# Optimization experiments

Hardware: AMD Instinct MI355X
Metric: run time of the kernel (lower is better)

Reference implementation:

```python
import jax, jax.numpy as jnp
import numpy as np

EMBED = 2048
HEADS = 16
HEAD_DIM = EMBED // HEADS


def setup_inputs() -> dict:
    key = jax.random.key(0)
    ks = jax.random.split(key, 9)
    s = 1.0 / np.sqrt(EMBED)
    inp = {"x": jax.random.normal(ks[0], (2, 2048, EMBED), dtype=jnp.float32)}
    for i, name in enumerate(["q", "k", "v", "o"]):
        inp[f"W{name}"] = jax.random.uniform(ks[1 + 2 * i], (EMBED, EMBED), dtype=jnp.float32, minval=-s, maxval=s)
        inp[f"b{name}"] = jax.random.uniform(ks[2 + 2 * i], (EMBED,), dtype=jnp.float32, minval=-s, maxval=s)
    return inp


def reference(x, Wq, bq, Wk, bk, Wv, bv, Wo, bo):
    B, S, E = x.shape
    def split_heads(t):
        return t.reshape(B, S, HEADS, HEAD_DIM).transpose(0, 2, 1, 3)  # [B,H,S,D]
    q = split_heads(x @ Wq.T + bq)
    k = split_heads(x @ Wk.T + bk)
    v = split_heads(x @ Wv.T + bv)
    scale = 1.0 / np.sqrt(HEAD_DIM)
    scores = jnp.einsum("bhqd,bhkd->bhqk", q, k) * scale  # [B,H,S,S]
    causal = jnp.tril(jnp.ones((S, S), dtype=bool))
    scores = jnp.where(causal[None, None], scores, -jnp.inf)
    attn = jax.nn.softmax(scores, axis=-1)
    out = jnp.einsum("bhqk,bhkd->bhqd", attn, v)  # [B,H,S,D]
    out = out.transpose(0, 2, 1, 3).reshape(B, S, E)
    return out @ Wo.T + bo
```

## Files before the change

### kernel.cpp

```cpp
#include <hip/hip_runtime.h>

typedef unsigned short u16;
typedef unsigned int u32;
typedef __attribute__((ext_vector_type(8))) short bf16x8;
typedef __attribute__((ext_vector_type(4))) float f32x4;

#define MFMA(a, b, c) __builtin_amdgcn_mfma_f32_16x16x32_bf16((a), (b), (c), 0, 0, 0)

__device__ inline u16 f2bf(float f) {
  u32 u = __float_as_uint(f);
  u = (u + 0x7fffu + ((u >> 16) & 1u)) >> 16;
  return (u16)u;
}

__device__ inline void gld16(u16* lds, const u16* g) {
  __builtin_amdgcn_global_load_lds((const __attribute__((address_space(1))) void*)g,
                                   (__attribute__((address_space(3))) void*)lds,
                                   16, 0, 0);
}

__global__ __launch_bounds__(256) void cvt_all(const float* __restrict__ x,
                                               const float* __restrict__ wa,
                                               const float* __restrict__ wb,
                                               const float* __restrict__ wc,
                                               const float* __restrict__ wd,
                                               uint2* __restrict__ dst) {
  int i = blockIdx.x * 256 + threadIdx.x;
  const float* s;
  int off;
  if (i < 2097152) {
    s = x; off = i;
  } else {
    int j = i - 2097152;
    int which = j >> 20;
    off = j & 1048575;
    s = (which == 0) ? wa : (which == 1) ? wb : (which == 2) ? wc : wd;
  }
  float4 f = ((const float4*)s)[off];
  u32 lo = (u32)f2bf(f.x) | ((u32)f2bf(f.y) << 16);
  u32 hi = (u32)f2bf(f.z) | ((u32)f2bf(f.w) << 16);
  dst[i] = make_uint2(lo, hi);
}

__device__ inline void gemm_core(const u16* __restrict__ A, const u16* __restrict__ W,
                                 u16* As, u16* Bs, int m0, int n0, f32x4 acc[4][4]) {
  const int K = 2048;
  const int NT = 64;
  int t = threadIdx.x, w = t >> 6, l = t & 63;
  int wr = (w >> 1) * 64, wc = (w & 1) * 64;
  int fr = l & 15, fg = l >> 4;
  int r0 = t >> 2;
  int r1 = 64 + r0;
  int c00 = (t & 3) ^ ((r0 >> 1) & 3);
  int c01 = (t & 3) ^ ((r1 >> 1) & 3);
  const u16* gA = A + (size_t)m0 * K;
  const u16* gB = W + (size_t)n0 * K;
  size_t a0 = (size_t)r0 * K + c00 * 8;
  size_t a1 = (size_t)r1 * K + c01 * 8;
#pragma unroll
  for (int p = 0; p < 2; ++p) {
    u16* sa = As + p * 4096;
    u16* sb = Bs + p * 4096;
    int kk = p * 32;
    gld16(sa + w * 512, gA + a0 + kk);
    gld16(sa + 2048 + w * 512, gA + a1 + kk);
    gld16(sb + w * 512, gB + a0 + kk);
    gld16(sb + 2048 + w * 512, gB + a1 + kk);
  }
  for (int kt = 0; kt < NT; ++kt) {
    int kt2 = (kt + 2 < NT) ? (kt + 2) : (NT - 1);
    u16* sa = As + ((kt + 2) & 3) * 4096;
    u16* sb = Bs + ((kt + 2) & 3) * 4096;
    int kk = kt2 * 32;
    gld16(sa + w * 512, gA + a0 + kk);
    gld16(sa + 2048 + w * 512, gA + a1 + kk);
    gld16(sb + w * 512, gB + a0 + kk);
    gld16(sb + 2048 + w * 512, gB + a1 + kk);
    asm volatile("s_waitcnt vmcnt(8)\n\ts_barrier" ::: "memory");
    const u16* ca = As + (kt & 3) * 4096;
    const u16* cb = Bs + (kt & 3) * 4096;
    bf16x8 af[4], bfv[4];
#pragma unroll
    for (int i = 0; i < 4; ++i) {
      int ar = wr + i * 16 + fr;
      af[i] = *(const bf16x8*)&ca[ar * 32 + ((fg ^ ((ar >> 1) & 3)) << 3)];
    }
#pragma unroll
    for (int i = 0; i < 4; ++i) {
      int br = wc + i * 16 + fr;
      bfv[i] = *(const bf16x8*)&cb[br * 32 + ((fg ^ ((br >> 1) & 3)) << 3)];
    }
    __builtin_amdgcn_s_setprio(1);
#pragma unroll
    for (int mi = 0; mi < 4; ++mi)
#pragma unroll
      for (int ni = 0; ni < 4; ++ni)
        acc[mi][ni] = MFMA(af[mi], bfv[ni], acc[mi][ni]);
    __builtin_amdgcn_s_setprio(0);
  }
}

__global__ __launch_bounds__(512, 2) void qk_gemm(
    const u16* __restrict__ X, const u16* __restrict__ Wq, const u16* __restrict__ Wk,
    const float* __restrict__ bq, const float* __restrict__ bk, u16* __restrict__ Qo,
    u16* __restrict__ Ko) {
  __shared__ __attribute__((aligned(16))) u16 As[32768];
  __shared__ __attribute__((aligned(16))) u16 Bs[32768];
  const int K = 2048, NT = 64;
  int which = blockIdx.x >> 3;
  int n0 = (blockIdx.x & 7) * 256;
  int m0 = blockIdx.y * 256;
  const u16* W = (which == 0) ? Wq : Wk;
  const float* bias = (which == 0) ? bq : bk;
  u16* out = (which == 0) ? Qo : Ko;
  float scale = (which == 0) ? 0.08838834764831845f : 1.0f;
  int t = threadIdx.x, w = t >> 6, l = t & 63;
  int wm = w >> 2, wn = w & 3;
  int fr = l & 15, fg = l >> 4;
  int r0 = t >> 2;
  int c0 = (t & 3) ^ ((r0 >> 1) & 3);
  const u16* gA = X + (size_t)m0 * K;
  const u16* gB = W + (size_t)n0 * K;
  size_t a0 = (size_t)r0 * K + c0 * 8;
  size_t a1 = a0 + (size_t)128 * K;
  f32x4 zero4 = {0.f, 0.f, 0.f, 0.f};
  f32x4 acc[8][4];
#pragma unroll
  for (int i = 0; i < 8; ++i)
#pragma unroll
    for (int j = 0; j < 4; ++j) acc[i][j] = zero4;
#pragma unroll
  for (int p = 0; p < 2; ++p) {
    u16* sa = As + p * 8192;
    u16* sb = Bs + p * 8192;
    int kk = p * 32;
    gld16(sa + w * 512, gA + a0 + kk);
    gld16(sa + 4096 + w * 512, gA + a1 + kk);
    gld16(sb + w * 512, gB + a0 + kk);
    gld16(sb + 4096 + w * 512, gB + a1 + kk);
  }
  for (int kt = 0; kt < NT; ++kt) {
    int kt2 = (kt + 2 < NT) ? (kt + 2) : (NT - 1);
    u16* sa = As + ((kt + 2) & 3) * 8192;
    u16* sb = Bs + ((kt + 2) & 3) * 8192;
    int kk = kt2 * 32;
    gld16(sa + w * 512, gA + a0 + kk);
    gld16(sa + 4096 + w * 512, gA + a1 + kk);
    gld16(sb + w * 512, gB + a0 + kk);
    gld16(sb + 4096 + w * 512, gB + a1 + kk);
    asm volatile("s_waitcnt vmcnt(8)\n\ts_barrier" ::: "memory");
    const u16* ca = As + (kt & 3) * 8192;
    const u16* cb = Bs + (kt & 3) * 8192;
    bf16x8 af[8], bfv[4];
#pragma unroll
    for (int i = 0; i < 8; ++i) {
      int ar = wm * 128 + i * 16 + fr;
      af[i] = *(const bf16x8*)&ca[ar * 32 + ((fg ^ ((ar >> 1) & 3)) << 3)];
    }
#pragma unroll
    for (int i = 0; i < 4; ++i) {
      int br = wn * 64 + i * 16 + fr;
      bfv[i] = *(const bf16x8*)&cb[br * 32 + ((fg ^ ((br >> 1) & 3)) << 3)];
    }
    __builtin_amdgcn_s_setprio(1);
#pragma unroll
    for (int mi = 0; mi < 8; ++mi)
#pragma unroll
      for (int ni = 0; ni < 4; ++ni)
        acc[mi][ni] = MFMA(af[mi], bfv[ni], acc[mi][ni]);
    __builtin_amdgcn_s_setprio(0);
  }
#pragma unroll
  for (int mi = 0; mi < 8; ++mi) {
#pragma unroll
    for (int ni = 0; ni < 4; ++ni) {
      int row = m0 + wm * 128 + mi * 16 + (l >> 4) * 4;
      int col = n0 + wn * 64 + ni * 16 + (l & 15);
      float bb = bias[col];
      int h = col >> 7, d = col & 127;
#pragma unroll
      for (int i = 0; i < 4; ++i) {
        int m = row + i;
        int b = m >> 11, s = m & 2047;
        float v = (acc[mi][ni][i] + bb) * scale;
        out[(((size_t)b * 16 + h) * 2048 + s) * 128 + d] = f2bf(v);
      }
    }
  }
}

__global__ __launch_bounds__(256, 2) void v_gemm(const u16* __restrict__ X,
                                                 const u16* __restrict__ Wv,
                                                 const float* __restrict__ bv,
                                                 u16* __restrict__ Vo) {
  __shared__ __attribute__((aligned(16))) u16 As[16384];
  __shared__ __attribute__((aligned(16))) u16 Bs[16384];
  int n0 = blockIdx.x * 128, m0 = blockIdx.y * 128;
  f32x4 zero4 = {0.f, 0.f, 0.f, 0.f};
  f32x4 acc[4][4];
#pragma unroll
  for (int i = 0; i < 4; ++i)
#pragma unroll
    for (int j = 0; j < 4; ++j) acc[i][j] = zero4;
  gemm_core(X, Wv, As, Bs, m0, n0, acc);
  int t = threadIdx.x, w = t >> 6, l = t & 63;
  int wr = (w >> 1) * 64, wc = (w & 1) * 64;
#pragma unroll
  for (int mi = 0; mi < 4; ++mi) {
#pragma unroll
    for (int ni = 0; ni < 4; ++ni) {
      int row = m0 + wr + mi * 16 + (l >> 4) * 4;
      int col = n0 + wc + ni * 16 + (l & 15);
      float bb = bv[col];
      int h = col >> 7, d = col & 127;
      int b = row >> 11, s = row & 2047;
      u32 p0 = (u32)f2bf(acc[mi][ni][0] + bb) | ((u32)f2bf(acc[mi][ni][1] + bb) << 16);
      u32 p1 = (u32)f2bf(acc[mi][ni][2] + bb) | ((u32)f2bf(acc[mi][ni][3] + bb) << 16);
      *(uint2*)&Vo[((size_t)(b * 16 + h) * 128 + d) * 2048 + s] = make_uint2(p0, p1);
    }
  }
}

__global__ __launch_bounds__(256, 2) void oproj_gemm(const u16* __restrict__ A,
                                                     const u16* __restrict__ W,
                                                     const float* __restrict__ bias,
                                                     float* __restrict__ out) {
  __shared__ __attribute__((aligned(16))) u16 As[16384];
  __shared__ __attribute__((aligned(16))) u16 Bs[16384];
  int n0 = blockIdx.x * 128, m0 = blockIdx.y * 128;
  f32x4 zero4 = {0.f, 0.f, 0.f, 0.f};
  f32x4 acc[4][4];
#pragma unroll
  for (int i = 0; i < 4; ++i)
#pragma unroll
    for (int j = 0; j < 4; ++j) acc[i][j] = zero4;
  gemm_core(A, W, As, Bs, m0, n0, acc);
  int t = threadIdx.x, w = t >> 6, l = t & 63;
  int wr = (w >> 1) * 64, wc = (w & 1) * 64;
#pragma unroll
  for (int mi = 0; mi < 4; ++mi) {
#pragma unroll
    for (int ni = 0; ni < 4; ++ni) {
      int row = m0 + wr + mi * 16 + (l >> 4) * 4;
      int col = n0 + wc + ni * 16 + (l & 15);
      float bb = bias[col];
#pragma unroll
      for (int i = 0; i < 4; ++i) out[(size_t)(row + i) * 2048 + col] = acc[mi][ni][i] + bb;
    }
  }
}

__global__ __launch_bounds__(256, 2) void attn_fwd(const u16* __restrict__ Q,
                                                   const u16* __restrict__ K,
                                                   const u16* __restrict__ Vt,
                                                   u16* __restrict__ AO) {
  __shared__ __attribute__((aligned(16))) u16 Ks[16384];
  __shared__ __attribute__((aligned(16))) u16 Vts[16384];
  __shared__ __attribute__((aligned(16))) u16 Pl[8192];
  const int D = 128;
  int b3 = blockIdx.x;
  int bh = b3 & 31;
  int xq = b3 >> 5;
  int qt = (xq < 8) ? (15 - xq) : (xq - 8);
  int t = threadIdx.x, w = t >> 6, l = t & 63, g = l >> 4, c = l & 15;
  size_t base = (size_t)bh * 2048 * 128;
  const u16* Vbh = Vt + base;
  int q0 = qt * 128;
  int qrw = q0 + w * 32;
  bf16x8 qf[2][4];
#pragma unroll
  for (int mi = 0; mi < 2; ++mi) {
    const u16* qp = Q + base + (size_t)(qrw + mi * 16 + c) * D + g * 8;
#pragma unroll
    for (int ks = 0; ks < 4; ++ks) qf[mi][ks] = *(const bf16x8*)(qp + ks * 32);
  }
  f32x4 zero4 = {0.f, 0.f, 0.f, 0.f};
  f32x4 oacc[2][8];
#pragma unroll
  for (int mi = 0; mi < 2; ++mi)
#pragma unroll
    for (int i = 0; i < 8; ++i) oacc[mi][i] = zero4;
  float mrow[2][4], lrow[2][4];
#pragma unroll
  for (int mi = 0; mi < 2; ++mi)
#pragma unroll
    for (int i = 0; i < 4; ++i) { mrow[mi][i] = -1e30f; lrow[mi][i] = 0.f; }
  char* pw = (char*)(Pl + w * 2048);
  int ktmax = 2 * qt + 1;
#define STAGE_TILE(BUF, KV0)                                                          \
  {                                                                                   \
    _Pragma("unroll") for (int ci = 0; ci < 4; ++ci) {                                \
      int row = w * 16 + ci * 4 + g;                                                  \
      int cc = c ^ (row & 7);                                                         \
      gld16(Ks + (BUF)*8192 + w * 2048 + ci * 512,                                    \
            K + base + (size_t)((KV0) + row) * D + cc * 8);                           \
    }                                                                                 \
    _Pragma("unroll") for (int ci = 0; ci < 4; ++ci) {                                \
      int vr = ci * 32 + w * 8 + (l >> 3);                                            \
      int vslot = (l & 7) ^ ((l >> 3) & 7);                                           \
      gld16(Vts + (BUF)*8192 + ci * 2048 + w * 512,                                   \
            Vbh + (size_t)vr * 2048 + (KV0) + vslot * 8);                             \
    }                                                                                 \
  }
  STAGE_TILE(0, 0)
  for (int kt = 0; kt <= ktmax; ++kt) {
    int kv0 = kt * 64;
    int ktn = (kt + 1 <= ktmax) ? (kt + 1) : ktmax;
    STAGE_TILE((kt + 1) & 1, ktn * 64)
    asm volatile("s_waitcnt vmcnt(8)\n\ts_barrier" ::: "memory");
    const u16* Kb = Ks + (kt & 1) * 8192;
    const u16* Vb2 = Vts + (kt & 1) * 8192;
    if (kv0 <= qrw + 31) {
      f32x4 sacc[2][4];
#pragma unroll
      for (int mi = 0; mi < 2; ++mi)
#pragma unroll
        for (int n = 0; n < 4; ++n) sacc[mi][n] = zero4;
#pragma unroll
      for (int ks = 0; ks < 4; ++ks) {
#pragma unroll
        for (int n = 0; n < 4; ++n) {
          int row = n * 16 + c;
          bf16x8 kf = *(const bf16x8*)&Kb[row * 128 + (((ks * 4 + g) ^ (c & 7)) << 3)];
          sacc[0][n] = MFMA(qf[0][ks], kf, sacc[0][n]);
          sacc[1][n] = MFMA(qf[1][ks], kf, sacc[1][n]);
        }
      }
      float sc[2][4][4];
#pragma unroll
      for (int mi = 0; mi < 2; ++mi)
#pragma unroll
        for (int n = 0; n < 4; ++n)
#pragma unroll
          for (int i = 0; i < 4; ++i) sc[mi][n][i] = sacc[mi][n][i];
      if (kv0 + 63 > qrw) {
#pragma unroll
        for (int mi = 0; mi < 2; ++mi)
#pragma unroll
          for (int n = 0; n < 4; ++n) {
            int kv = kv0 + n * 16 + c;
#pragma unroll
            for (int i = 0; i < 4; ++i)
              if (kv > qrw + mi * 16 + g * 4 + i) sc[mi][n][i] = -1e30f;
          }
      }
      float tmax[2][4];
#pragma unroll
      for (int mi = 0; mi < 2; ++mi)
#pragma unroll
        for (int i = 0; i < 4; ++i)
          tmax[mi][i] = fmaxf(fmaxf(sc[mi][0][i], sc[mi][1][i]), fmaxf(sc[mi][2][i], sc[mi][3][i]));
#pragma unroll
      for (int x = 1; x < 16; x <<= 1)
#pragma unroll
        for (int mi = 0; mi < 2; ++mi)
#pragma unroll
          for (int i = 0; i < 4; ++i) tmax[mi][i] = fmaxf(tmax[mi][i], __shfl_xor(tmax[mi][i], x));
      float corr[2][4], rs[2][4];
#pragma unroll
      for (int mi = 0; mi < 2; ++mi)
#pragma unroll
        for (int i = 0; i < 4; ++i) {
          float mn = fmaxf(mrow[mi][i], tmax[mi][i]);
          corr[mi][i] = __expf(mrow[mi][i] - mn);
          mrow[mi][i] = mn;
          rs[mi][i] = 0.f;
        }
      float ps[2][4][4];
#pragma unroll
      for (int mi = 0; mi < 2; ++mi)
#pragma unroll
        for (int n = 0; n < 4; ++n)
#pragma unroll
          for (int i = 0; i < 4; ++i) {
            ps[mi][n][i] = __expf(sc[mi][n][i] - mrow[mi][i]);
            rs[mi][i] += ps[mi][n][i];
          }
#pragma unroll
      for (int x = 1; x < 16; x <<= 1)
#pragma unroll
        for (int mi = 0; mi < 2; ++mi)
#pragma unroll
          for (int i = 0; i < 4; ++i) rs[mi][i] += __shfl_xor(rs[mi][i], x);
#pragma unroll
      for (int mi = 0; mi < 2; ++mi)
#pragma unroll
        for (int i = 0; i < 4; ++i) lrow[mi][i] = lrow[mi][i] * corr[mi][i] + rs[mi][i];
#pragma unroll
      for (int mi = 0; mi < 2; ++mi)
#pragma unroll
        for (int nf = 0; nf < 8; ++nf)
#pragma unroll
          for (int i = 0; i < 4; ++i) oacc[mi][nf][i] *= corr[mi][i];
#pragma unroll
      for (int mi = 0; mi < 2; ++mi)
#pragma unroll
        for (int n = 0; n < 4; ++n)
#pragma unroll
          for (int i = 0; i < 4; ++i) {
            int row = mi * 16 + g * 4 + i;
            *(u16*)(pw + row * 128 + ((n * 32 + c * 2) ^ ((row & 7) << 4))) = f2bf(ps[mi][n][i]);
          }
#pragma unroll
      for (int ks = 0; ks < 2; ++ks) {
        bf16x8 pf0 = *(const bf16x8*)(pw + (c)*128 + ((ks * 64 + g * 16) ^ ((c & 7) << 4)));
        bf16x8 pf1 = *(const bf16x8*)(pw + (16 + c) * 128 + ((ks * 64 + g * 16) ^ ((c & 7) << 4)));
#pragma unroll
        for (int nf = 0; nf < 8; ++nf) {
          bf16x8 vf = *(const bf16x8*)&Vb2[(nf * 16 + c) * 64 + (((ks * 4 + g) ^ (c & 7)) << 3)];
          oacc[0][nf] = MFMA(pf0, vf, oacc[0][nf]);
          oacc[1][nf] = MFMA(pf1, vf, oacc[1][nf]);
        }
      }
    }
    __syncthreads();
  }
  int b = bh >> 4, h = bh & 15;
#pragma unroll
  for (int mi = 0; mi < 2; ++mi)
#pragma unroll
    for (int nf = 0; nf < 8; ++nf) {
      int d = h * 128 + nf * 16 + c;
#pragma unroll
      for (int i = 0; i < 4; ++i) {
        int q = qrw + mi * 16 + g * 4 + i;
        AO[((size_t)b * 2048 + q) * 2048 + d] = f2bf(oacc[mi][nf][i] / lrow[mi][i]);
      }
    }
}

extern "C" void kernel_launch(void* const* d_in, const int* in_sizes, int n_in,
                              void* d_out, int out_size, void* d_ws, size_t ws_size,
                              hipStream_t stream) {
  const float* x = (const float*)d_in[0];
  const float* Wq = (const float*)d_in[1];
  const float* bq = (const float*)d_in[2];
  const float* Wk = (const float*)d_in[3];
  const float* bk = (const float*)d_in[4];
  const float* Wv = (const float*)d_in[5];
  const float* bv = (const float*)d_in[6];
  const float* Wo = (const float*)d_in[7];
  const float* bo = (const float*)d_in[8];
  float* out = (float*)d_out;

  u16* xb = (u16*)d_ws;
  u16* Wqb = xb + 8388608;
  u16* Wkb = Wqb + 4194304;
  u16* Wvb = Wkb + 4194304;
  u16* Wob = Wvb + 4194304;
  u16* Qb = Wob + 4194304;
  u16* Kb = Qb + 8388608;
  u16* Vb = Kb + 8388608;
  u16* AOb = xb;

  cvt_all<<<24576, 256, 0, stream>>>(x, Wq, Wk, Wv, Wo, (uint2*)d_ws);
  qk_gemm<<<dim3(16, 16), 512, 0, stream>>>(xb, Wqb, Wkb, bq, bk, Qb, Kb);
  v_gemm<<<dim3(16, 32), 256, 0, stream>>>(xb, Wvb, bv, Vb);
  attn_fwd<<<512, 256, 0, stream>>>(Qb, Kb, Vb, AOb);
  oproj_gemm<<<dim3(16, 32), 256, 0, stream>>>(AOb, Wob, bo, out);
}
```

Measured before the change: 278.7 us.

## Single-buffer attention K/V tiles for higher occupancy, use exp2 and lazy rescaling

The attention kernel drops double-buffered K/V staging in LDS for a single buffer loaded between two barriers. This cuts shared memory per block enough to allow three blocks per CU, up from two, and launch bounds are raised to match. The log2(e) factor is folded into the Q projection scale so softmax can use exp2f directly. Output and row-sum rescaling is skipped unless some row's max grows by more than 8 in log2 units (wave-wide vote). The cost is that K/V loads no longer overlap with compute inside a block, so the design relies on the extra resident blocks to hide that latency.

```diff
diff --git a/kernel.cpp b/kernel.cpp
--- a/kernel.cpp
+++ b/kernel.cpp
@@ -113,7 +113,7 @@
   const u16* W = (which == 0) ? Wq : Wk;
   const float* bias = (which == 0) ? bq : bk;
   u16* out = (which == 0) ? Qo : Ko;
-  float scale = (which == 0) ? 0.08838834764831845f : 1.0f;
+  float scale = (which == 0) ? 0.08838834764831845f * 1.4426950408889634f : 1.0f;
   int t = threadIdx.x, w = t >> 6, l = t & 63;
   int wm = w >> 2, wn = w & 3;
   int fr = l & 15, fg = l >> 4;
@@ -250,12 +250,12 @@
   }
 }
 
-__global__ __launch_bounds__(256, 2) void attn_fwd(const u16* __restrict__ Q,
+__global__ __launch_bounds__(256, 3) void attn_fwd(const u16* __restrict__ Q,
                                                    const u16* __restrict__ K,
                                                    const u16* __restrict__ Vt,
                                                    u16* __restrict__ AO) {
-  __shared__ __attribute__((aligned(16))) u16 Ks[16384];
-  __shared__ __attribute__((aligned(16))) u16 Vts[16384];
+  __shared__ __attribute__((aligned(16))) u16 Ks[8192];
+  __shared__ __attribute__((aligned(16))) u16 Vts[8192];
   __shared__ __attribute__((aligned(16))) u16 Pl[8192];
   const int D = 128;
   int b3 = blockIdx.x;
@@ -287,29 +287,22 @@
     for (int i = 0; i < 4; ++i) { mrow[mi][i] = -1e30f; lrow[mi][i] = 0.f; }
   char* pw = (char*)(Pl + w * 2048);
   int ktmax = 2 * qt + 1;
-#define STAGE_TILE(BUF, KV0)                                                          \
-  {                                                                                   \
-    _Pragma("unroll") for (int ci = 0; ci < 4; ++ci) {                                \
-      int row = w * 16 + ci * 4 + g;                                                  \
-      int cc = c ^ (row & 7);                                                         \
-      gld16(Ks + (BUF)*8192 + w * 2048 + ci * 512,                                    \
-            K + base + (size_t)((KV0) + row) * D + cc * 8);                           \
-    }                                                                                 \
-    _Pragma("unroll") for (int ci = 0; ci < 4; ++ci) {                                \
-      int vr = ci * 32 + w * 8 + (l >> 3);                                            \
-      int vslot = (l & 7) ^ ((l >> 3) & 7);                                           \
-      gld16(Vts + (BUF)*8192 + ci * 2048 + w * 512,                                   \
-            Vbh + (size_t)vr * 2048 + (KV0) + vslot * 8);                             \
-    }                                                                                 \
-  }
-  STAGE_TILE(0, 0)
   for (int kt = 0; kt <= ktmax; ++kt) {
     int kv0 = kt * 64;
-    int ktn = (kt + 1 <= ktmax) ? (kt + 1) : ktmax;
-    STAGE_TILE((kt + 1) & 1, ktn * 64)
-    asm volatile("s_waitcnt vmcnt(8)\n\ts_barrier" ::: "memory");
-    const u16* Kb = Ks + (kt & 1) * 8192;
-    const u16* Vb2 = Vts + (kt & 1) * 8192;
+    __syncthreads();
+#pragma unroll
+    for (int ci = 0; ci < 4; ++ci) {
+      int row = w * 16 + ci * 4 + g;
+      int cc = c ^ (row & 7);
+      gld16(Ks + w * 2048 + ci * 512, K + base + (size_t)(kv0 + row) * D + cc * 8);
+    }
+#pragma unroll
+    for (int ci = 0; ci < 4; ++ci) {
+      int vr = ci * 32 + w * 8 + (l >> 3);
+      int vslot = (l & 7) ^ ((l >> 3) & 7);
+      gld16(Vts + ci * 2048 + w * 512, Vbh + (size_t)vr * 2048 + kv0 + vslot * 8);
+    }
+    __syncthreads();
     if (kv0 <= qrw + 31) {
       f32x4 sacc[2][4];
 #pragma unroll
@@ -321,7 +314,7 @@
 #pragma unroll
         for (int n = 0; n < 4; ++n) {
           int row = n * 16 + c;
-          bf16x8 kf = *(const bf16x8*)&Kb[row * 128 + (((ks * 4 + g) ^ (c & 7)) << 3)];
+          bf16x8 kf = *(const bf16x8*)&Ks[row * 128 + (((ks * 4 + g) ^ (c & 7)) << 3)];
           sacc[0][n] = MFMA(qf[0][ks], kf, sacc[0][n]);
           sacc[1][n] = MFMA(qf[1][ks], kf, sacc[1][n]);
         }
@@ -356,24 +349,36 @@
         for (int mi = 0; mi < 2; ++mi)
 #pragma unroll
           for (int i = 0; i < 4; ++i) tmax[mi][i] = fmaxf(tmax[mi][i], __shfl_xor(tmax[mi][i], x));
-      float corr[2][4], rs[2][4];
-#pragma unroll
-      for (int mi = 0; mi < 2; ++mi)
-#pragma unroll
-        for (int i = 0; i < 4; ++i) {
-          float mn = fmaxf(mrow[mi][i], tmax[mi][i]);
-          corr[mi][i] = __expf(mrow[mi][i] - mn);
-          mrow[mi][i] = mn;
-          rs[mi][i] = 0.f;
-        }
-      float ps[2][4][4];
+      bool over = false;
+#pragma unroll
+      for (int mi = 0; mi < 2; ++mi)
+#pragma unroll
+        for (int i = 0; i < 4; ++i) over = over || (tmax[mi][i] > mrow[mi][i] + 8.0f);
+      if (__any(over)) {
+#pragma unroll
+        for (int mi = 0; mi < 2; ++mi)
+#pragma unroll
+          for (int i = 0; i < 4; ++i) {
+            float mn = fmaxf(mrow[mi][i], tmax[mi][i]);
+            float corr = exp2f(mrow[mi][i] - mn);
+            mrow[mi][i] = mn;
+            lrow[mi][i] *= corr;
+#pragma unroll
+            for (int nf = 0; nf < 8; ++nf) oacc[mi][nf][i] *= corr;
+          }
+      }
+      float ps[2][4][4], rs[2][4];
+#pragma unroll
+      for (int mi = 0; mi < 2; ++mi)
+#pragma unroll
+        for (int i = 0; i < 4; ++i) rs[mi][i] = 0.f;
 #pragma unroll
       for (int mi = 0; mi < 2; ++mi)
 #pragma unroll
         for (int n = 0; n < 4; ++n)
 #pragma unroll
           for (int i = 0; i < 4; ++i) {
-            ps[mi][n][i] = __expf(sc[mi][n][i] - mrow[mi][i]);
+            ps[mi][n][i] = exp2f(sc[mi][n][i] - mrow[mi][i]);
             rs[mi][i] += ps[mi][n][i];
           }
 #pragma unroll
@@ -385,13 +390,7 @@
 #pragma unroll
       for (int mi = 0; mi < 2; ++mi)
 #pragma unroll
-        for (int i = 0; i < 4; ++i) lrow[mi][i] = lrow[mi][i] * corr[mi][i] + rs[mi][i];
-#pragma unroll
-      for (int mi = 0; mi < 2; ++mi)
-#pragma unroll
-        for (int nf = 0; nf < 8; ++nf)
-#pragma unroll
-          for (int i = 0; i < 4; ++i) oacc[mi][nf][i] *= corr[mi][i];
+        for (int i = 0; i < 4; ++i) lrow[mi][i] += rs[mi][i];
 #pragma unroll
       for (int mi = 0; mi < 2; ++mi)
 #pragma unroll
@@ -407,13 +406,12 @@
         bf16x8 pf1 = *(const bf16x8*)(pw + (16 + c) * 128 + ((ks * 64 + g * 16) ^ ((c & 7) << 4)));
 #pragma unroll
         for (int nf = 0; nf < 8; ++nf) {
-          bf16x8 vf = *(const bf16x8*)&Vb2[(nf * 16 + c) * 64 + (((ks * 4 + g) ^ (c & 7)) << 3)];
+          bf16x8 vf = *(const bf16x8*)&Vts[(nf * 16 + c) * 64 + (((ks * 4 + g) ^ (c & 7)) << 3)];
           oacc[0][nf] = MFMA(pf0, vf, oacc[0][nf]);
           oacc[1][nf] = MFMA(pf1, vf, oacc[1][nf]);
         }
       }
     }
-    __syncthreads();
   }
   int b = bh >> 4, h = bh & 15;
 #pragma unroll
```

After: 460.9 us. 1.65x slower.

## Split attention query tile across eight waves of sixteen rows each

Applied to the files above, without the earlier changes.

The attention kernel now runs 512 threads per block, with each of eight waves owning 16 query rows instead of four waves owning 32. The tile staging, P scratch layout and wait counts are rebalanced to match. The aim is more waves to hide latency, and less per-wave causal imbalance, with fewer registers per wave. In exchange each K/V fragment read from LDS feeds only one MFMA instead of two, which doubles LDS read traffic per unit of compute.

```diff
diff --git a/kernel.cpp b/kernel.cpp
--- a/kernel.cpp
+++ b/kernel.cpp
@@ -250,7 +250,7 @@
   }
 }
 
-__global__ __launch_bounds__(256, 2) void attn_fwd(const u16* __restrict__ Q,
+__global__ __launch_bounds__(512, 4) void attn_fwd(const u16* __restrict__ Q,
                                                    const u16* __restrict__ K,
                                                    const u16* __restrict__ Vt,
                                                    u16* __restrict__ AO) {
@@ -266,39 +266,34 @@
   size_t base = (size_t)bh * 2048 * 128;
   const u16* Vbh = Vt + base;
   int q0 = qt * 128;
-  int qrw = q0 + w * 32;
-  bf16x8 qf[2][4];
-#pragma unroll
-  for (int mi = 0; mi < 2; ++mi) {
-    const u16* qp = Q + base + (size_t)(qrw + mi * 16 + c) * D + g * 8;
-#pragma unroll
-    for (int ks = 0; ks < 4; ++ks) qf[mi][ks] = *(const bf16x8*)(qp + ks * 32);
+  int qrw = q0 + w * 16;
+  bf16x8 qf[4];
+  {
+    const u16* qp = Q + base + (size_t)(qrw + c) * D + g * 8;
+#pragma unroll
+    for (int ks = 0; ks < 4; ++ks) qf[ks] = *(const bf16x8*)(qp + ks * 32);
   }
   f32x4 zero4 = {0.f, 0.f, 0.f, 0.f};
-  f32x4 oacc[2][8];
-#pragma unroll
-  for (int mi = 0; mi < 2; ++mi)
-#pragma unroll
-    for (int i = 0; i < 8; ++i) oacc[mi][i] = zero4;
-  float mrow[2][4], lrow[2][4];
-#pragma unroll
-  for (int mi = 0; mi < 2; ++mi)
-#pragma unroll
-    for (int i = 0; i < 4; ++i) { mrow[mi][i] = -1e30f; lrow[mi][i] = 0.f; }
-  char* pw = (char*)(Pl + w * 2048);
+  f32x4 oacc[8];
+#pragma unroll
+  for (int i = 0; i < 8; ++i) oacc[i] = zero4;
+  float mrow[4], lrow[4];
+#pragma unroll
+  for (int i = 0; i < 4; ++i) { mrow[i] = -1e30f; lrow[i] = 0.f; }
+  char* pw = (char*)(Pl + w * 1024);
   int ktmax = 2 * qt + 1;
 #define STAGE_TILE(BUF, KV0)                                                          \
   {                                                                                   \
-    _Pragma("unroll") for (int ci = 0; ci < 4; ++ci) {                                \
-      int row = w * 16 + ci * 4 + g;                                                  \
-      int cc = c ^ (row & 7);                                                         \
-      gld16(Ks + (BUF)*8192 + w * 2048 + ci * 512,                                    \
+    _Pragma("unroll") for (int i = 0; i < 2; ++i) {                                   \
+      int row = i * 32 + w * 4 + (l >> 4);                                            \
+      int cc = (l & 15) ^ (row & 7);                                                  \
+      gld16(Ks + (BUF)*8192 + i * 4096 + w * 512,                                     \
             K + base + (size_t)((KV0) + row) * D + cc * 8);                           \
     }                                                                                 \
-    _Pragma("unroll") for (int ci = 0; ci < 4; ++ci) {                                \
-      int vr = ci * 32 + w * 8 + (l >> 3);                                            \
+    _Pragma("unroll") for (int i = 0; i < 2; ++i) {                                   \
+      int vr = i * 64 + w * 8 + (l >> 3);                                             \
       int vslot = (l & 7) ^ ((l >> 3) & 7);                                           \
-      gld16(Vts + (BUF)*8192 + ci * 2048 + w * 512,                                   \
+      gld16(Vts + (BUF)*8192 + i * 4096 + w * 512,                                    \
             Vbh + (size_t)vr * 2048 + (KV0) + vslot * 8);                             \
     }                                                                                 \
   }
@@ -307,109 +302,84 @@
     int kv0 = kt * 64;
     int ktn = (kt + 1 <= ktmax) ? (kt + 1) : ktmax;
     STAGE_TILE((kt + 1) & 1, ktn * 64)
-    asm volatile("s_waitcnt vmcnt(8)\n\ts_barrier" ::: "memory");
+    asm volatile("s_waitcnt vmcnt(4)\n\ts_barrier" ::: "memory");
     const u16* Kb = Ks + (kt & 1) * 8192;
     const u16* Vb2 = Vts + (kt & 1) * 8192;
-    if (kv0 <= qrw + 31) {
-      f32x4 sacc[2][4];
-#pragma unroll
-      for (int mi = 0; mi < 2; ++mi)
-#pragma unroll
-        for (int n = 0; n < 4; ++n) sacc[mi][n] = zero4;
+    if (kv0 <= qrw + 15) {
+      f32x4 sacc[4];
+#pragma unroll
+      for (int n = 0; n < 4; ++n) sacc[n] = zero4;
 #pragma unroll
       for (int ks = 0; ks < 4; ++ks) {
 #pragma unroll
         for (int n = 0; n < 4; ++n) {
           int row = n * 16 + c;
           bf16x8 kf = *(const bf16x8*)&Kb[row * 128 + (((ks * 4 + g) ^ (c & 7)) << 3)];
-          sacc[0][n] = MFMA(qf[0][ks], kf, sacc[0][n]);
-          sacc[1][n] = MFMA(qf[1][ks], kf, sacc[1][n]);
+          sacc[n] = MFMA(qf[ks], kf, sacc[n]);
         }
       }
-      float sc[2][4][4];
-#pragma unroll
-      for (int mi = 0; mi < 2; ++mi)
-#pragma unroll
-        for (int n = 0; n < 4; ++n)
-#pragma unroll
-          for (int i = 0; i < 4; ++i) sc[mi][n][i] = sacc[mi][n][i];
+      float sc[4][4];
+#pragma unroll
+      for (int n = 0; n < 4; ++n)
+#pragma unroll
+        for (int i = 0; i < 4; ++i) sc[n][i] = sacc[n][i];
       if (kv0 + 63 > qrw) {
 #pragma unroll
-        for (int mi = 0; mi < 2; ++mi)
-#pragma unroll
-          for (int n = 0; n < 4; ++n) {
-            int kv = kv0 + n * 16 + c;
-#pragma unroll
-            for (int i = 0; i < 4; ++i)
-              if (kv > qrw + mi * 16 + g * 4 + i) sc[mi][n][i] = -1e30f;
-          }
+        for (int n = 0; n < 4; ++n) {
+          int kv = kv0 + n * 16 + c;
+#pragma unroll
+          for (int i = 0; i < 4; ++i)
+            if (kv > qrw + g * 4 + i) sc[n][i] = -1e30f;
+        }
       }
-      float tmax[2][4];
-#pragma unroll
-      for (int mi = 0; mi < 2; ++mi)
-#pragma unroll
-        for (int i = 0; i < 4; ++i)
-          tmax[mi][i] = fmaxf(fmaxf(sc[mi][0][i], sc[mi][1][i]), fmaxf(sc[mi][2][i], sc[mi][3][i]));
+      float tmax[4];
+#pragma unroll
+      for (int i = 0; i < 4; ++i)
+        tmax[i] = fmaxf(fmaxf(sc[0][i], sc[1][i]), fmaxf(sc[2][i], sc[3][i]));
 #pragma unroll
       for (int x = 1; x < 16; x <<= 1)
 #pragma unroll
-        for (int mi = 0; mi < 2; ++mi)
-#pragma unroll
-          for (int i = 0; i < 4; ++i) tmax[mi][i] = fmaxf(tmax[mi][i], __shfl_xor(tmax[mi][i], x));
-      float corr[2][4], rs[2][4];
-#pragma unroll
-      for (int mi = 0; mi < 2; ++mi)
+        for (int i = 0; i < 4; ++i) tmax[i] = fmaxf(tmax[i], __shfl_xor(tmax[i], x));
+      float corr[4], rs[4];
+#pragma unroll
+      for (int i = 0; i < 4; ++i) {
+        float mn = fmaxf(mrow[i], tmax[i]);
+        corr[i] = __expf(mrow[i] - mn);
+        mrow[i] = mn;
+        rs[i] = 0.f;
+      }
+      float ps[4][4];
+#pragma unroll
+      for (int n = 0; n < 4; ++n)
 #pragma unroll
         for (int i = 0; i < 4; ++i) {
-          float mn = fmaxf(mrow[mi][i], tmax[mi][i]);
-          corr[mi][i] = __expf(mrow[mi][i] - mn);
-          mrow[mi][i] = mn;
-          rs[mi][i] = 0.f;
+          ps[n][i] = __expf(sc[n][i] - mrow[i]);
+          rs[i] += ps[n][i];
         }
-      float ps[2][4][4];
-#pragma unroll
-      for (int mi = 0; mi < 2; ++mi)
-#pragma unroll
-        for (int n = 0; n < 4; ++n)
-#pragma unroll
-          for (int i = 0; i < 4; ++i) {
-            ps[mi][n][i] = __expf(sc[mi][n][i] - mrow[mi][i]);
-            rs[mi][i] += ps[mi][n][i];
-          }
 #pragma unroll
       for (int x = 1; x < 16; x <<= 1)
 #pragma unroll
-        for (int mi = 0; mi < 2; ++mi)
-#pragma unroll
-          for (int i = 0; i < 4; ++i) rs[mi][i] += __shfl_xor(rs[mi][i], x);
-#pragma unroll
-      for (int mi = 0; mi < 2; ++mi)
-#pragma unroll
-        for (int i = 0; i < 4; ++i) lrow[mi][i] = lrow[mi][i] * corr[mi][i] + rs[mi][i];
-#pragma unroll
-      for (int mi = 0; mi < 2; ++mi)
-#pragma unroll
-        for (int nf = 0; nf < 8; ++nf)
-#pragma unroll
-          for (int i = 0; i < 4; ++i) oacc[mi][nf][i] *= corr[mi][i];
-#pragma unroll
-      for (int mi = 0; mi < 2; ++mi)
-#pragma unroll
-        for (int n = 0; n < 4; ++n)
-#pragma unroll
-          for (int i = 0; i < 4; ++i) {
-            int row = mi * 16 + g * 4 + i;
-            *(u16*)(pw + row * 128 + ((n * 32 + c * 2) ^ ((row & 7) << 4))) = f2bf(ps[mi][n][i]);
-          }
+        for (int i = 0; i < 4; ++i) rs[i] += __shfl_xor(rs[i], x);
+#pragma unroll
+      for (int i = 0; i < 4; ++i) lrow[i] = lrow[i] * corr[i] + rs[i];
+#pragma unroll
+      for (int nf = 0; nf < 8; ++nf)
+#pragma unroll
+        for (int i = 0; i < 4; ++i) oacc[nf][i] *= corr[i];
+#pragma unroll
+      for (int n = 0; n < 4; ++n)
+#pragma unroll
+        for (int i = 0; i < 4; ++i) {
+          int row = g * 4 + i;
+          *(u16*)(pw + row * 128 + ((n * 32 + c * 2) ^ ((row & 7) << 4))) = f2bf(ps[n][i]);
+        }
 #pragma unroll
       for (int ks = 0; ks < 2; ++ks) {
-        bf16x8 pf0 = *(const bf16x8*)(pw + (c)*128 + ((ks * 64 + g * 16) ^ ((c & 7) << 4)));
-        bf16x8 pf1 = *(const bf16x8*)(pw + (16 + c) * 128 + ((ks * 64 + g * 16) ^ ((c & 7) << 4)));
+        bf16x8 pf = *(const bf16x8*)(pw + c * 128 + ((ks * 64 + g * 16) ^ ((c & 7) << 4)));
 #pragma unroll
         for (int nf = 0; nf < 8; ++nf) {
           bf16x8 vf = *(const bf16x8*)&Vb2[(nf * 16 + c) * 64 + (((ks * 4 + g) ^ (c & 7)) << 3)];
-          oacc[0][nf] = MFMA(pf0, vf, oacc[0][nf]);
-          oacc[1][nf] = MFMA(pf1, vf, oacc[1][nf]);
+          oacc[nf] = MFMA(pf, vf, oacc[nf]);
         }
       }
     }
@@ -417,16 +387,14 @@
   }
   int b = bh >> 4, h = bh & 15;
 #pragma unroll
-  for (int mi = 0; mi < 2; ++mi)
-#pragma unroll
-    for (int nf = 0; nf < 8; ++nf) {
-      int d = h * 128 + nf * 16 + c;
-#pragma unroll
-      for (int i = 0; i < 4; ++i) {
-        int q = qrw + mi * 16 + g * 4 + i;
-        AO[((size_t)b * 2048 + q) * 2048 + d] = f2bf(oacc[mi][nf][i] / lrow[mi][i]);
-      }
-    }
+  for (int nf = 0; nf < 8; ++nf) {
+    int d = h * 128 + nf * 16 + c;
+#pragma unroll
+    for (int i = 0; i < 4; ++i) {
+      int q = qrw + g * 4 + i;
+      AO[((size_t)b * 2048 + q) * 2048 + d] = f2bf(oacc[nf][i] / lrow[i]);
+    }
+  }
 }
 
 extern "C" void kernel_launch(void* const* d_in, const int* in_sizes, int n_in,
@@ -456,6 +424,6 @@
   cvt_all<<<24576, 256, 0, stream>>>(x, Wq, Wk, Wv, Wo, (uint2*)d_ws);
   qk_gemm<<<dim3(16, 16), 512, 0, stream>>>(xb, Wqb, Wkb, bq, bk, Qb, Kb);
   v_gemm<<<dim3(16, 32), 256, 0, stream>>>(xb, Wvb, bv, Vb);
-  attn_fwd<<<512, 256, 0, stream>>>(Qb, Kb, Vb, AOb);
+  attn_fwd<<<512, 512, 0, stream>>>(Qb, Kb, Vb, AOb);
   oproj_gemm<<<dim3(16, 32), 256, 0, stream>>>(AOb, Wob, bo, out);
 }
```

Measured after the change: 275.9 us. No clear change (-1.0%).
